# Kernel optimization log

Measured on AMD Instinct MI355X. Metric: run time of the kernel, lower is better.

## Reference

```python
import jax, jax.numpy as jnp
import numpy as np


def setup_inputs() -> dict:
    key = jax.random.key(0)
    k1, k2, k3 = jax.random.split(key, 3)
    B, C, D, S = 16, 80, 1024, 14  # batch, num_classes, feature dim, conv size
    return {
        "batch_size": B,
        "img_feature_map": jax.random.normal(k1, (B, D, S, S), dtype=jnp.float32),
        "word_features": jax.random.normal(k2, (C, D), dtype=jnp.float32),
        "fc_a_w": jax.random.normal(k3, (D,), dtype=jnp.float32) / np.float32(np.sqrt(D)),
        "fc_a_b": jnp.zeros((), dtype=jnp.float32),
    }


def reference(batch_size, img_feature_map, word_features, fc_a_w, fc_a_b):
    # img_feature_map: [B, D, H, W] -> [B, H, W, D]
    img = jnp.transpose(img_feature_map, (0, 2, 3, 1))
    # class-wise gated feature: tanh(img * word) -> [B, H, W, C, D]
    gated = jnp.tanh(img[:, :, :, None, :] * word_features[None, None, None, :, :])
    # rank-1 linear score: [B, H, W, C]
    scores = jnp.einsum('bhwcd,d->bhwc', gated, fc_a_w) + fc_a_b
    B, H, W, C = scores.shape
    # softmax over spatial positions (H*W) per (batch, class)
    coef = jax.nn.softmax(scores.reshape(B, H * W, C), axis=1).reshape(B, H, W, C)
    # attention-weighted spatial pooling -> [B, C, D]
    return jnp.einsum('bhwc,bhwd->bcd', coef, img)
```

## Files before the change

kernel.cpp:

```cpp
#include <hip/hip_runtime.h>

#define BB 16
#define CC 80
#define DD 1024
#define HW 196
#define NSP (BB * HW)
#define NCH 8
#define DCH 128
#define NCQ 16
#define CPB 5
#define TWO_LOG2E 2.8853900817779268f

__global__ __launch_bounds__(256) void scores_k(const float* __restrict__ img,
                                                const float* __restrict__ word,
                                                const float* __restrict__ fa,
                                                float* __restrict__ partial) {
    const int g = blockIdx.x * 256 + threadIdx.x;
    if (g >= NSP) return;
    const int b  = g / HW;
    const int hw = g - b * HW;
    const int d0 = blockIdx.y * DCH;
    const int c0 = blockIdx.z * CPB;

    const float* ip = img + ((size_t)b * DD + d0) * HW + hw;

    float p[CPB];
#pragma unroll
    for (int k = 0; k < CPB; ++k) p[k] = 0.f;

    for (int q = 0; q < DCH / 32; ++q) {
        float iv[32];
#pragma unroll
        for (int i = 0; i < 32; ++i)
            iv[i] = ip[(size_t)(q * 32 + i) * HW] * TWO_LOG2E;

        const float* fp = fa + d0 + q * 32;
        float fv[32];
#pragma unroll
        for (int i = 0; i < 32; ++i) fv[i] = fp[i];

#pragma unroll
        for (int k = 0; k < CPB; ++k) {
            const float* wp = word + (size_t)(c0 + k) * DD + d0 + q * 32;
            float p0 = 0.f, p1 = 0.f;
#pragma unroll
            for (int i = 0; i < 32; i += 2) {
                float y0 = iv[i]     * wp[i];
                float y1 = iv[i + 1] * wp[i + 1];
                float e0 = __builtin_amdgcn_exp2f(y0);
                float e1 = __builtin_amdgcn_exp2f(y1);
                float r0 = __builtin_amdgcn_rcpf(e0 + 1.f);
                float r1 = __builtin_amdgcn_rcpf(e1 + 1.f);
                p0 = fmaf(fv[i],     r0, p0);
                p1 = fmaf(fv[i + 1], r1, p1);
            }
            p[k] += p0 + p1;
        }
    }

#pragma unroll
    for (int k = 0; k < CPB; ++k)
        partial[(((size_t)b * NCH + blockIdx.y) * CC + (c0 + k)) * HW + hw] = p[k];
}

__global__ __launch_bounds__(256) void softmax_k(const float* __restrict__ partial,
                                                 float* __restrict__ coef) {
    const int bc = blockIdx.x;
    const int b = bc / CC, c = bc - b * CC;
    const int t = threadIdx.x;

    float P = 0.f;
    if (t < HW) {
#pragma unroll
        for (int ch = 0; ch < NCH; ++ch)
            P += partial[(((size_t)b * NCH + ch) * CC + c) * HW + t];
    }
    float x = (t < HW) ? (-TWO_LOG2E) * P : -3.4e38f;

    __shared__ float rmax[4], rsum[4];
    const int wv = t >> 6;

    float m = x;
#pragma unroll
    for (int off = 32; off >= 1; off >>= 1) m = fmaxf(m, __shfl_xor(m, off, 64));
    if ((t & 63) == 0) rmax[wv] = m;
    __syncthreads();
    m = fmaxf(fmaxf(rmax[0], rmax[1]), fmaxf(rmax[2], rmax[3]));

    float e = (t < HW) ? __builtin_amdgcn_exp2f(x - m) : 0.f;
    float s = e;
#pragma unroll
    for (int off = 32; off >= 1; off >>= 1) s += __shfl_xor(s, off, 64);
    if ((t & 63) == 0) rsum[wv] = s;
    __syncthreads();
    s = rsum[0] + rsum[1] + rsum[2] + rsum[3];

    if (t < HW) coef[((size_t)b * CC + c) * HW + t] = e * __builtin_amdgcn_rcpf(s);
}

__global__ __launch_bounds__(512) void pool_k(const float* __restrict__ img,
                                              const float* __restrict__ coef,
                                              float* __restrict__ out) {
    __shared__ float it[64 * HW];
    const int b  = blockIdx.x;
    const int d0 = blockIdx.y * 64;
    const int t  = threadIdx.x;

    const float4* src = (const float4*)(img + ((size_t)b * DD + d0) * HW);
    float4* dst = (float4*)it;
    for (int j = t; j < 64 * HW / 4; j += 512) dst[j] = src[j];
    __syncthreads();

    const int w = t >> 6, l = t & 63;
    const float* irow = it + l * HW;
    const int cbase = w * 10;
    const float* cb = coef + ((size_t)b * CC + cbase) * HW;

    float acc[10];
#pragma unroll
    for (int k = 0; k < 10; ++k) acc[k] = 0.f;

    for (int h = 0; h < HW; h += 4) {
        float4 ivv = *(const float4*)(irow + h);
#pragma unroll
        for (int k = 0; k < 10; ++k) {
            const float* crow = cb + (size_t)k * HW + h;
            acc[k] = fmaf(crow[0], ivv.x, acc[k]);
            acc[k] = fmaf(crow[1], ivv.y, acc[k]);
            acc[k] = fmaf(crow[2], ivv.z, acc[k]);
            acc[k] = fmaf(crow[3], ivv.w, acc[k]);
        }
    }

#pragma unroll
    for (int k = 0; k < 10; ++k)
        out[((size_t)b * CC + cbase + k) * DD + d0 + l] = acc[k];
}

extern "C" void kernel_launch(void* const* d_in, const int* in_sizes, int n_in,
                              void* d_out, int out_size, void* d_ws, size_t ws_size,
                              hipStream_t stream) {
    const float* img  = (const float*)d_in[1];
    const float* word = (const float*)d_in[2];
    const float* fa   = (const float*)d_in[3];
    float* out = (float*)d_out;

    float* partial = (float*)d_ws;
    float* coef    = partial + (size_t)BB * NCH * CC * HW;

    scores_k<<<dim3((NSP + 255) / 256, NCH, NCQ), 256, 0, stream>>>(img, word, fa, partial);
    softmax_k<<<BB * CC, 256, 0, stream>>>(partial, coef);
    pool_k<<<dim3(BB, DD / 64), 512, 0, stream>>>(img, coef, out);
}
```

Baseline: 166.1 us.

## Double-buffer image loads in scores kernel and tile pool over class groups

The scores kernel now loads the next 32-element slice of image values into a second register buffer before computing on the current one, so load latency overlaps with the exp/rcp math. fa is read directly instead of being staged into a register array. The pool kernel gains a class-group grid dimension and stages both the image tile and a 16-class slice of coefficients in shared memory, with each thread accumulating 4 classes. This raises parallelism and cuts repeated global coefficient reads, but each block now reloads the 64-channel image tile once per class group and uses more shared memory and registers.

```diff
diff --git a/kernel.cpp b/kernel.cpp
--- a/kernel.cpp
+++ b/kernel.cpp
@@ -9,6 +9,7 @@
 #define DCH 128
 #define NCQ 16
 #define CPB 5
+#define PCL 16
 #define TWO_LOG2E 2.8853900817779268f
 
 __global__ __launch_bounds__(256) void scores_k(const float* __restrict__ img,
@@ -28,17 +29,16 @@
 #pragma unroll
     for (int k = 0; k < CPB; ++k) p[k] = 0.f;
 
-    for (int q = 0; q < DCH / 32; ++q) {
-        float iv[32];
+    float ivA[32], ivB[32];
+
+    auto loadq = [&](float* iv, int q) {
+        const float* qp = ip + (size_t)q * 32 * HW;
 #pragma unroll
         for (int i = 0; i < 32; ++i)
-            iv[i] = ip[(size_t)(q * 32 + i) * HW] * TWO_LOG2E;
-
+            iv[i] = qp[(size_t)i * HW] * TWO_LOG2E;
+    };
+    auto compute = [&](const float* iv, int q) {
         const float* fp = fa + d0 + q * 32;
-        float fv[32];
-#pragma unroll
-        for (int i = 0; i < 32; ++i) fv[i] = fp[i];
-
 #pragma unroll
         for (int k = 0; k < CPB; ++k) {
             const float* wp = word + (size_t)(c0 + k) * DD + d0 + q * 32;
@@ -51,12 +51,21 @@
                 float e1 = __builtin_amdgcn_exp2f(y1);
                 float r0 = __builtin_amdgcn_rcpf(e0 + 1.f);
                 float r1 = __builtin_amdgcn_rcpf(e1 + 1.f);
-                p0 = fmaf(fv[i],     r0, p0);
-                p1 = fmaf(fv[i + 1], r1, p1);
+                p0 = fmaf(fp[i],     r0, p0);
+                p1 = fmaf(fp[i + 1], r1, p1);
             }
             p[k] += p0 + p1;
         }
-    }
+    };
+
+    loadq(ivA, 0);
+    loadq(ivB, 1);
+    compute(ivA, 0);
+    loadq(ivA, 2);
+    compute(ivB, 1);
+    loadq(ivB, 3);
+    compute(ivA, 2);
+    compute(ivB, 3);
 
 #pragma unroll
     for (int k = 0; k < CPB; ++k)
@@ -98,43 +107,47 @@
     if (t < HW) coef[((size_t)b * CC + c) * HW + t] = e * __builtin_amdgcn_rcpf(s);
 }
 
-__global__ __launch_bounds__(512) void pool_k(const float* __restrict__ img,
+__global__ __launch_bounds__(256) void pool_k(const float* __restrict__ img,
                                               const float* __restrict__ coef,
                                               float* __restrict__ out) {
     __shared__ float it[64 * HW];
+    __shared__ float ct[PCL * HW];
     const int b  = blockIdx.x;
     const int d0 = blockIdx.y * 64;
+    const int cg = blockIdx.z * PCL;
     const int t  = threadIdx.x;
 
     const float4* src = (const float4*)(img + ((size_t)b * DD + d0) * HW);
     float4* dst = (float4*)it;
-    for (int j = t; j < 64 * HW / 4; j += 512) dst[j] = src[j];
+    for (int j = t; j < 64 * HW / 4; j += 256) dst[j] = src[j];
+    const float4* csrc = (const float4*)(coef + ((size_t)b * CC + cg) * HW);
+    float4* cdst = (float4*)ct;
+    for (int j = t; j < PCL * HW / 4; j += 256) cdst[j] = csrc[j];
     __syncthreads();
 
-    const int w = t >> 6, l = t & 63;
-    const float* irow = it + l * HW;
-    const int cbase = w * 10;
-    const float* cb = coef + ((size_t)b * CC + cbase) * HW;
+    const int d  = t & 63;
+    const int cq = t >> 6;
+    const float* irow = it + d * HW;
+    const float* crow = ct + (cq * 4) * HW;
 
-    float acc[10];
-#pragma unroll
-    for (int k = 0; k < 10; ++k) acc[k] = 0.f;
-
+    float a0 = 0.f, a1 = 0.f, a2 = 0.f, a3 = 0.f;
     for (int h = 0; h < HW; h += 4) {
-        float4 ivv = *(const float4*)(irow + h);
-#pragma unroll
-        for (int k = 0; k < 10; ++k) {
-            const float* crow = cb + (size_t)k * HW + h;
-            acc[k] = fmaf(crow[0], ivv.x, acc[k]);
-            acc[k] = fmaf(crow[1], ivv.y, acc[k]);
-            acc[k] = fmaf(crow[2], ivv.z, acc[k]);
-            acc[k] = fmaf(crow[3], ivv.w, acc[k]);
-        }
+        float4 iv  = *(const float4*)(irow + h);
+        float4 c0v = *(const float4*)(crow + h);
+        float4 c1v = *(const float4*)(crow + HW + h);
+        float4 c2v = *(const float4*)(crow + 2 * HW + h);
+        float4 c3v = *(const float4*)(crow + 3 * HW + h);
+        a0 = fmaf(iv.x, c0v.x, fmaf(iv.y, c0v.y, fmaf(iv.z, c0v.z, fmaf(iv.w, c0v.w, a0))));
+        a1 = fmaf(iv.x, c1v.x, fmaf(iv.y, c1v.y, fmaf(iv.z, c1v.z, fmaf(iv.w, c1v.w, a1))));
+        a2 = fmaf(iv.x, c2v.x, fmaf(iv.y, c2v.y, fmaf(iv.z, c2v.z, fmaf(iv.w, c2v.w, a2))));
+        a3 = fmaf(iv.x, c3v.x, fmaf(iv.y, c3v.y, fmaf(iv.z, c3v.z, fmaf(iv.w, c3v.w, a3))));
     }
 
-#pragma unroll
-    for (int k = 0; k < 10; ++k)
-        out[((size_t)b * CC + cbase + k) * DD + d0 + l] = acc[k];
+    float* op = out + ((size_t)b * CC + cg + cq * 4) * DD + d0 + d;
+    op[0]      = a0;
+    op[DD]     = a1;
+    op[2 * DD] = a2;
+    op[3 * DD] = a3;
 }
 
 extern "C" void kernel_launch(void* const* d_in, const int* in_sizes, int n_in,
@@ -150,5 +163,5 @@
 
     scores_k<<<dim3((NSP + 255) / 256, NCH, NCQ), 256, 0, stream>>>(img, word, fa, partial);
     softmax_k<<<BB * CC, 256, 0, stream>>>(partial, coef);
-    pool_k<<<dim3(BB, DD / 64), 512, 0, stream>>>(img, coef, out);
+    pool_k<<<dim3(BB, DD / 64, CC / PCL), 256, 0, stream>>>(img, coef, out);
 }
```

Result: no change. 162.9 us (-1.9%).
